# Kernel tuning notes

Measured on AMD Instinct MI355X. Metric: run time of the kernel, lower is better.

## Reference

```python
import jax, jax.numpy as jnp
import numpy as np

EPS_NORM = 1e-12
BN_EPS = 1e-5
TEMP = 0.07


def _l2norm(x, axis):
    n = jnp.sqrt(jnp.sum(x * x, axis=axis, keepdims=True))
    return x / jnp.maximum(n, EPS_NORM)


def _bn_eval(z, w, b):
    # inference-mode BatchNorm2d with running_mean=0, running_var=1
    s = w / jnp.sqrt(jnp.asarray(1.0 + BN_EPS, z.dtype))
    return z * s[None, :, None, None] + b[None, :, None, None]


def setup_inputs() -> dict:
    key = jax.random.key(0)
    ks = jax.random.split(key, 8)
    B, C, H, W = 16, 256, 64, 64
    KD, P = 128, 256
    x = jax.random.normal(ks[0], (B, C, H, W), jnp.float32)
    m_features = jax.random.normal(ks[1], (P, KD), jnp.float32)
    q_w = jax.random.normal(ks[2], (KD, C), jnp.float32) * 0.05
    k_w = jax.random.normal(ks[3], (KD, KD), jnp.float32) * 0.05
    v_w = jax.random.normal(ks[4], (KD, KD), jnp.float32) * 0.05
    o_w = jax.random.normal(ks[5], (C, KD), jnp.float32) * 0.05
    dw_w = jax.random.normal(ks[6], (C, 1, 3, 3), jnp.float32) * 0.1
    return {
        "x": x, "m_features": m_features,
        "q_w": q_w, "q_b": jnp.zeros((KD,), jnp.float32),
        "k_w": k_w, "k_b": jnp.zeros((KD,), jnp.float32),
        "v_w": v_w, "v_b": jnp.zeros((KD,), jnp.float32),
        "o_w": o_w, "o_b": jnp.zeros((C,), jnp.float32),
        "dw_w": dw_w,
        "bn1_w": jnp.ones((C,), jnp.float32), "bn1_b": jnp.zeros((C,), jnp.float32),
        "bn2_w": jnp.ones((C,), jnp.float32), "bn2_b": jnp.zeros((C,), jnp.float32),
        "gamma": jnp.ones((C,), jnp.float32) * 1e-5,
    }


def reference(x, m_features, q_w, q_b, k_w, k_b, v_w, v_b, o_w, o_b,
              dw_w, bn1_w, bn1_b, bn2_w, bn2_b, gamma):
    B, C, H, W = x.shape
    KD = q_w.shape[0]
    residual = x
    # q_proj 1x1 conv -> [B,KD,H,W], L2-normalize over channel dim
    q = jnp.einsum('bchw,kc->bkhw', x, q_w) + q_b[None, :, None, None]
    q = _l2norm(q, axis=1)
    q = q.reshape(B, KD, H * W).transpose(0, 2, 1)  # [B, HW, KD]
    # k/v projections of memory bank [P, KD]
    k = _l2norm(m_features @ k_w.T + k_b, axis=-1)
    v = m_features @ v_w.T + v_b
    # fp32 attention with clamped logits
    q32, k32, v32 = q.astype(jnp.float32), k.astype(jnp.float32), v.astype(jnp.float32)
    logits = jnp.clip(jnp.einsum('bnd,pd->bnp', q32, k32) / TEMP, -30.0, 30.0)
    attn = jax.nn.softmax(logits, axis=-1)
    out = jnp.einsum('bnp,pd->bnd', attn, v32).astype(x.dtype)
    out = out.transpose(0, 2, 1).reshape(B, KD, H, W)
    # out_proj 1x1 conv -> [B,C,H,W]
    out = jnp.einsum('bkhw,ck->bchw', out, o_w) + o_b[None, :, None, None]
    # local branch: depthwise 3x3 conv + BN + exact GELU
    local = jax.lax.conv_general_dilated(
        out, dw_w, window_strides=(1, 1), padding='SAME',
        feature_group_count=C,
        dimension_numbers=('NCHW', 'OIHW', 'NCHW'))
    local = jax.nn.gelu(_bn_eval(local, bn1_w, bn1_b), approximate=False)
    out = out + local
    return _bn_eval(residual + out * gamma[None, :, None, None], bn2_w, bn2_b)
```

## Files before the change

### kernel.cpp

```cpp
#include <hip/hip_runtime.h>
#include <hip/hip_bf16.h>
#include <math.h>

#define B_ 16
#define C_ 256
#define H_ 64
#define W_ 64
#define KD_ 128
#define P_ 256
#define HW_ (H_ * W_)

typedef __bf16 bf16;
typedef bf16 bf16x8_t __attribute__((ext_vector_type(8)));
typedef float f32x4_t __attribute__((ext_vector_type(4)));
typedef float f32x16_t __attribute__((ext_vector_type(16)));
typedef unsigned char u8;

__device__ __forceinline__ unsigned cvt_pk_fp8_lo(float a, float b, unsigned old) {
#if __has_builtin(__builtin_amdgcn_cvt_pk_fp8_f32)
    return __builtin_amdgcn_cvt_pk_fp8_f32(a, b, old, false);
#else
    unsigned r = old;
    asm("v_cvt_pk_fp8_f32 %0, %1, %2" : "+v"(r) : "v"(a), "v"(b));
    return r;
#endif
}
__device__ __forceinline__ unsigned cvt_pk_fp8_hi(float a, float b, unsigned old) {
#if __has_builtin(__builtin_amdgcn_cvt_pk_fp8_f32)
    return __builtin_amdgcn_cvt_pk_fp8_f32(a, b, old, true);
#else
    unsigned r = old;
    asm("v_cvt_pk_fp8_f32 %0, %1, %2 op_sel:[0,0,1]" : "+v"(r) : "v"(a), "v"(b));
    return r;
#endif
}
__device__ __forceinline__ uint2 pack8_fp8(const float* f) {
    uint2 r;
    r.x = cvt_pk_fp8_hi(f[2], f[3], cvt_pk_fp8_lo(f[0], f[1], 0u));
    r.y = cvt_pk_fp8_hi(f[6], f[7], cvt_pk_fp8_lo(f[4], f[5], 0u));
    return r;
}

__global__ __launch_bounds__(512, 8) void k_xpose(
    const float* __restrict__ x, u8* __restrict__ x8)
{
    __shared__ __align__(16) u8 tile[16 * 2048];
    const int cblk = blockIdx.x >> 1;
    const int ph   = blockIdx.x & 1;
    const int b    = blockIdx.y;
    const int t = threadIdx.x;

    {
        const int cl = t >> 5, sub = t & 31;
        const float* src = x + ((size_t)b * C_ + cblk * 16 + cl) * HW_ + ph * 2048;
#pragma unroll
        for (int i = 0; i < 16; ++i) {
            const f32x4_t v = *(const f32x4_t*)(src + (i * 32 + sub) * 4);
            const unsigned w = cvt_pk_fp8_hi(v[2], v[3],
                               cvt_pk_fp8_lo(v[0], v[1], 0u));
            *(unsigned*)&tile[cl * 2048 + (i * 32 + sub) * 4] = w;
        }
    }
    __syncthreads();

    {
        const int pr = t & 63;
        const int r0 = t >> 6;
#pragma unroll
        for (int it = 0; it < 4; ++it) {
            const int r = it * 8 + r0;
            const int lp = r * 64 + pr;
            union { u8 bytes[16]; uint4 u; } g;
#pragma unroll
            for (int c = 0; c < 16; ++c) g.bytes[c] = tile[c * 2048 + lp];
            const int h = ph * 32 + r;
            *(uint4*)(x8 + (((size_t)(b * 64 + h) * 16 + cblk) << 10) + pr * 16) = g.u;
        }
    }
}

__global__ __launch_bounds__(128) void k_prep1(
    const float* __restrict__ m_feat,
    const float* __restrict__ k_w, const float* __restrict__ k_b,
    const float* __restrict__ v_w, const float* __restrict__ v_b,
    float* __restrict__ kn_f, float* __restrict__ v_f)
{
    const int p = blockIdx.x;
    const int j = threadIdx.x;
    __shared__ float msh[KD_];
    __shared__ float red[2];
    msh[j] = m_feat[p * KD_ + j];
    __syncthreads();

    float ka = k_b[j];
    float va = v_b[j];
#pragma unroll 4
    for (int d = 0; d < KD_; ++d) {
        const float m = msh[d];
        ka = fmaf(m, k_w[j * KD_ + d], ka);
        va = fmaf(m, v_w[j * KD_ + d], va);
    }
    float s = ka * ka;
#pragma unroll
    for (int o = 1; o < 64; o <<= 1) s += __shfl_xor(s, o);
    if ((j & 63) == 0) red[j >> 6] = s;
    __syncthreads();
    s = red[0] + red[1];
    const float inv = 1.0f / (0.07f * fmaxf(sqrtf(s), 1e-12f));
    kn_f[p * KD_ + j] = ka * inv;
    v_f[p * KD_ + j] = va;
}

__global__ __launch_bounds__(256) void k_prep23(
    const float* __restrict__ o_w, const float* __restrict__ v_f,
    const float* __restrict__ q_w, const float* __restrict__ kn_f,
    u8* __restrict__ m28, u8* __restrict__ qw8, u8* __restrict__ kn8)
{
    if (blockIdx.x < 256) {
        const int c = blockIdx.x;
        const int p = threadIdx.x;
        __shared__ float osh[KD_];
        if (p < KD_) osh[p] = o_w[c * KD_ + p];
        __syncthreads();
        float acc = 0.f;
#pragma unroll 4
        for (int k = 0; k < KD_; ++k) acc = fmaf(osh[k], v_f[p * KD_ + k], acc);
        const int mt = c >> 5, r = c & 31;
        const int ks = p >> 4, sub = (p >> 3) & 1, jj = p & 7;
        const unsigned pk = cvt_pk_fp8_lo(acc * 16.0f, 0.f, 0u);
        m28[(((mt * 16 + ks) * 64) + sub * 32 + r) * 8 + jj] = (u8)(pk & 0xffu);
    } else {
        const int t = (blockIdx.x - 256) * 256 + threadIdx.x;
        float f[8];
        if (t < 4096) {
            const int lane = t & 63, g = t >> 6, mt = g >> 4, ks = g & 15;
            const int row = mt * 32 + (lane & 31), k0 = ks * 16 + (lane >> 5) * 8;
            const float* src = q_w + row * C_ + k0;
#pragma unroll
            for (int j = 0; j < 8; ++j) f[j] = src[j] * 16.0f;
            ((uint2*)qw8)[t] = pack8_fp8(f);
        } else {
            const int u = t - 4096;
            const int lane = u & 63, g = u >> 6, mt = g >> 3, ks = g & 7;
            const int row = mt * 32 + (lane & 31), k0 = ks * 16 + (lane >> 5) * 8;
            const float* src = kn_f + row * KD_ + k0;
#pragma unroll
            for (int j = 0; j < 8; ++j) f[j] = src[j];
            ((uint2*)kn8)[u] = pack8_fp8(f);
        }
    }
}

__global__ __launch_bounds__(512, 8) void k_attn(
    const u8* __restrict__ x8,
    const float* __restrict__ q_b, const float* __restrict__ o_b,
    const u8* __restrict__ qw8, const u8* __restrict__ kn8,
    const u8* __restrict__ m28, bf16* __restrict__ outf)
{
    __shared__ __align__(16) char lds[29696];
    char* const ebuf = lds;
    char* const qbuf = lds + 16384;
    float* const ss_lds   = (float*)(lds + 24576);
    float* const pmax_lds = (float*)(lds + 25600);
    float* const sum_lds  = (float*)(lds + 27648);

    const int h = blockIdx.x;
    const int b = blockIdx.y;
    const int tid = threadIdx.x;
    const int lane = tid & 63;
    const int wid = tid >> 6;
    const int l31 = lane & 31;
    const int kh  = lane >> 5;

    const int mtA = wid & 3, nhalf = wid >> 2;
    {
        const u8* xrow = x8 + ((size_t)(b * 64 + h) << 14);
        f32x16_t qacc;
#pragma unroll
        for (int i = 0; i < 16; ++i) qacc[i] = 0.f;
        const int pix = nhalf * 32 + l31;
#pragma unroll
        for (int ks = 0; ks < 16; ++ks) {
            const long a = *(const long*)(qw8 + ((mtA * 16 + ks) * 64 + lane) * 8);
            const long bx = *(const long*)(xrow + ks * 1024 + pix * 16 + kh * 8);
            qacc = __builtin_amdgcn_mfma_f32_32x32x16_fp8_fp8(a, bx, qacc, 0, 0, 0);
        }
        float ssp = 0.f;
#pragma unroll
        for (int g = 0; g < 4; ++g) {
            const f32x4_t qbv = *(const f32x4_t*)(q_b + mtA * 32 + g * 8 + kh * 4);
#pragma unroll
            for (int i = 0; i < 4; ++i) {
                const float qv = qacc[g * 4 + i] + 16.0f * qbv[i];
                qacc[g * 4 + i] = qv;
                ssp = fmaf(qv, qv, ssp);
            }
        }
        ssp += __shfl_xor(ssp, 32);
        if (lane < 32) ss_lds[pix * 4 + mtA] = ssp;
#pragma unroll
        for (int g = 0; g < 4; ++g) {
            const unsigned qw_ = cvt_pk_fp8_hi(qacc[g * 4 + 2], qacc[g * 4 + 3],
                                 cvt_pk_fp8_lo(qacc[g * 4 + 0], qacc[g * 4 + 1], 0u));
            *(unsigned*)(qbuf + pix * 128 +
                         ((mtA * 32 + g * 8 + kh * 4) ^ ((l31 & 15) << 3))) = qw_;
        }
    }
    __syncthreads();

    f32x16_t lacc0, lacc1;
#pragma unroll
    for (int i = 0; i < 16; ++i) { lacc0[i] = 0.f; lacc1[i] = 0.f; }
#pragma unroll
    for (int ks = 0; ks < 8; ++ks) {
        const long a = *(const long*)(kn8 + ((wid * 8 + ks) * 64 + lane) * 8);
        const long bq0 = *(const long*)(qbuf + (0 * 32 + l31) * 128 +
                                        ((ks * 16 + kh * 8) ^ ((l31 & 15) << 3)));
        const long bq1 = *(const long*)(qbuf + (1 * 32 + l31) * 128 +
                                        ((ks * 16 + kh * 8) ^ ((l31 & 15) << 3)));
        lacc0 = __builtin_amdgcn_mfma_f32_32x32x16_fp8_fp8(a, bq0, lacc0, 0, 0, 0);
        lacc1 = __builtin_amdgcn_mfma_f32_32x32x16_fp8_fp8(a, bq1, lacc1, 0, 0, 0);
    }
#pragma unroll
    for (int nt = 0; nt < 2; ++nt) {
        const int pix = nt * 32 + l31;
        float mx;
        if (nt == 0) {
            mx = lacc0[0];
#pragma unroll
            for (int i = 1; i < 16; ++i) mx = fmaxf(mx, lacc0[i]);
        } else {
            mx = lacc1[0];
#pragma unroll
            for (int i = 1; i < 16; ++i) mx = fmaxf(mx, lacc1[i]);
        }
        mx = fmaxf(mx, __shfl_xor(mx, 32));
        if (lane < 32) pmax_lds[pix * 8 + wid] = mx;
    }
    __syncthreads();

#pragma unroll
    for (int nt = 0; nt < 2; ++nt) {
        const int pix = nt * 32 + l31;
        const f32x4_t s4 = *(const f32x4_t*)(ss_lds + pix * 4);
        const float qinv = 1.0f / fmaxf(sqrtf(s4[0] + s4[1] + s4[2] + s4[3]), 1e-12f);
        const f32x4_t ma = *(const f32x4_t*)(pmax_lds + pix * 8);
        const f32x4_t mb = *(const f32x4_t*)(pmax_lds + pix * 8 + 4);
        const float cof = 5.545177444479562f -
                          fmaxf(fmaxf(fmaxf(ma[0], ma[1]), fmaxf(ma[2], ma[3])),
                                fmaxf(fmaxf(mb[0], mb[1]), fmaxf(mb[2], mb[3]))) * qinv;
        float sm = 0.f;
#pragma unroll
        for (int g = 0; g < 4; ++g) {
            float e[4];
#pragma unroll
            for (int i = 0; i < 4; ++i) {
                const float lv = (nt == 0) ? lacc0[g * 4 + i] : lacc1[g * 4 + i];
                e[i] = __expf(fmaf(lv, qinv, cof));
                sm += e[i];
            }
            const unsigned ew = cvt_pk_fp8_hi(e[2], e[3],
                                cvt_pk_fp8_lo(e[0], e[1], 0u));
            const int p0 = wid * 32 + g * 8 + kh * 4;
            *(unsigned*)(ebuf + pix * 256 + (p0 ^ (l31 << 3))) = ew;
        }
        sm += __shfl_xor(sm, 32);
        if (lane < 32) sum_lds[pix * 8 + wid] = sm;
    }
    __syncthreads();

    f32x16_t oacc0, oacc1;
#pragma unroll
    for (int i = 0; i < 16; ++i) { oacc0[i] = 0.f; oacc1[i] = 0.f; }
#pragma unroll
    for (int ks = 0; ks < 16; ++ks) {
        const long a = *(const long*)(m28 + ((wid * 16 + ks) * 64 + lane) * 8);
        const long be0 = *(const long*)(ebuf + (0 * 32 + l31) * 256 +
                                        ((ks * 16 + kh * 8) ^ (l31 << 3)));
        const long be1 = *(const long*)(ebuf + (1 * 32 + l31) * 256 +
                                        ((ks * 16 + kh * 8) ^ (l31 << 3)));
        oacc0 = __builtin_amdgcn_mfma_f32_32x32x16_fp8_fp8(a, be0, oacc0, 0, 0, 0);
        oacc1 = __builtin_amdgcn_mfma_f32_32x32x16_fp8_fp8(a, be1, oacc1, 0, 0, 0);
    }
    {
        const f32x4_t sa0 = *(const f32x4_t*)(sum_lds + (0 * 32 + l31) * 8);
        const f32x4_t sb0 = *(const f32x4_t*)(sum_lds + (0 * 32 + l31) * 8 + 4);
        const f32x4_t sa1 = *(const f32x4_t*)(sum_lds + (1 * 32 + l31) * 8);
        const f32x4_t sb1 = *(const f32x4_t*)(sum_lds + (1 * 32 + l31) * 8 + 4);
        const float rs0 = 1.0f / (16.0f * (sa0[0] + sa0[1] + sa0[2] + sa0[3] +
                                           sb0[0] + sb0[1] + sb0[2] + sb0[3]));
        const float rs1 = 1.0f / (16.0f * (sa1[0] + sa1[1] + sa1[2] + sa1[3] +
                                           sb1[0] + sb1[1] + sb1[2] + sb1[3]));
        bf16* const obase = outf + (size_t)b * C_ * HW_ + h * W_;
#pragma unroll
        for (int g = 0; g < 4; ++g) {
            const f32x4_t obv = *(const f32x4_t*)(o_b + wid * 32 + g * 8 + kh * 4);
#pragma unroll
            for (int i = 0; i < 4; ++i) {
                const int c = wid * 32 + g * 8 + kh * 4 + i;
                obase[(size_t)c * HW_ + l31]      = (bf16)fmaf(oacc0[g * 4 + i], rs0, obv[i]);
                obase[(size_t)c * HW_ + 32 + l31] = (bf16)fmaf(oacc1[g * 4 + i], rs1, obv[i]);
            }
        }
    }
}

__global__ __launch_bounds__(256) void k_post(
    const float* __restrict__ x, const bf16* __restrict__ outf,
    const float* __restrict__ dw_w,
    const float* __restrict__ bn1_w, const float* __restrict__ bn1_b,
    const float* __restrict__ bn2_w, const float* __restrict__ bn2_b,
    const float* __restrict__ gamma, float* __restrict__ y)
{
    __shared__ __align__(16) bf16 os[HW_];
    const int bc = blockIdx.x;
    const int c = bc & (C_ - 1);
    const int tid = threadIdx.x;

    const bf16* oc = outf + (size_t)bc * HW_;
#pragma unroll
    for (int it = 0; it < 2; ++it) {
        const int e = (it * 256 + tid) * 8;
        *(bf16x8_t*)&os[e] = *(const bf16x8_t*)&oc[e];
    }

    const float cbn = 0.99999500003750f;
    const float s1 = bn1_w[c] * cbn, b1 = bn1_b[c];
    const float s2 = bn2_w[c] * cbn, b2 = bn2_b[c];
    const float g = gamma[c];
    float kw[9];
#pragma unroll
    for (int j = 0; j < 9; ++j) kw[j] = dw_w[c * 9 + j];

    __syncthreads();

    const int w = tid & 63;
    const int h0 = (tid >> 6) * 16;

    float r0[3], r1[3], r2[3];
    auto ldrow = [&](int hh, float* r) {
        if ((unsigned)hh < (unsigned)H_) {
            r[1] = (float)os[hh * W_ + w];
            r[0] = (w > 0) ? (float)os[hh * W_ + w - 1] : 0.f;
            r[2] = (w < W_ - 1) ? (float)os[hh * W_ + w + 1] : 0.f;
        } else {
            r[0] = r[1] = r[2] = 0.f;
        }
    };
    ldrow(h0 - 1, r0);
    ldrow(h0, r1);

    const float* xc = x + (size_t)bc * HW_;
    float* yc = y + (size_t)bc * HW_;

#pragma unroll
    for (int i = 0; i < 16; ++i) {
        const int h = h0 + i;
        ldrow(h + 1, r2);
        float conv = kw[0] * r0[0];
        conv = fmaf(kw[1], r0[1], conv);
        conv = fmaf(kw[2], r0[2], conv);
        conv = fmaf(kw[3], r1[0], conv);
        conv = fmaf(kw[4], r1[1], conv);
        conv = fmaf(kw[5], r1[2], conv);
        conv = fmaf(kw[6], r2[0], conv);
        conv = fmaf(kw[7], r2[1], conv);
        conv = fmaf(kw[8], r2[2], conv);
        const float center = r1[1];
        const float t = fmaf(conv, s1, b1);
        const float lg = t / (1.0f + __expf(-1.702f * t));
        const int idx = h * W_ + w;
        yc[idx] = fmaf(center + lg, g, xc[idx]) * s2 + b2;
#pragma unroll
        for (int j = 0; j < 3; ++j) { r0[j] = r1[j]; r1[j] = r2[j]; }
    }
}

extern "C" void kernel_launch(void* const* d_in, const int* in_sizes, int n_in,
                              void* d_out, int out_size, void* d_ws, size_t ws_size,
                              hipStream_t stream)
{
    const float* x     = (const float*)d_in[0];
    const float* m_f   = (const float*)d_in[1];
    const float* q_w   = (const float*)d_in[2];
    const float* q_b   = (const float*)d_in[3];
    const float* k_w   = (const float*)d_in[4];
    const float* k_b   = (const float*)d_in[5];
    const float* v_w   = (const float*)d_in[6];
    const float* v_b   = (const float*)d_in[7];
    const float* o_w   = (const float*)d_in[8];
    const float* o_b   = (const float*)d_in[9];
    const float* dw_w  = (const float*)d_in[10];
    const float* bn1_w = (const float*)d_in[11];
    const float* bn1_b = (const float*)d_in[12];
    const float* bn2_w = (const float*)d_in[13];
    const float* bn2_b = (const float*)d_in[14];
    const float* gamma = (const float*)d_in[15];

    char* ws = (char*)d_ws;
    u8*    qw8   = (u8*)(ws);
    u8*    kn8   = (u8*)(ws + (32 << 10));
    u8*    m28   = (u8*)(ws + (64 << 10));
    u8*    x8    = (u8*)(ws + (1 << 20));
    bf16*  outf  = (bf16*)(ws + (17 << 20));
    float* kn_f  = (float*)(ws + (17 << 20));
    float* v_f   = (float*)(ws + (17 << 20) + (128 << 10));

    k_xpose<<<dim3(32, B_), dim3(512), 0, stream>>>(x, x8);
    k_prep1<<<dim3(P_), dim3(128), 0, stream>>>(m_f, k_w, k_b, v_w, v_b,
                                                kn_f, v_f);
    k_prep23<<<dim3(288), dim3(256), 0, stream>>>(o_w, v_f, q_w, kn_f,
                                                  m28, qw8, kn8);
    k_attn<<<dim3(H_, B_), dim3(512), 0, stream>>>(x8, q_b, o_b, qw8, kn8,
                                                   m28, outf);
    k_post<<<dim3(B_ * C_), dim3(256), 0, stream>>>(
        x, outf, dw_w, bn1_w, bn1_b, bn2_w, bn2_b, gamma, (float*)d_out);
}
```

Before: 87.09 us.

## Process two rows per attention block and pass fp8 intermediate to post kernel

The attention kernel now handles two image rows (128 pixels) per block, so each wave reuses its loaded K/V/weight fragments across four MFMA tiles instead of two, and the grid is halved. The attention output is stored as fp8, scaled by 16, instead of bf16, which halves the intermediate traffic. The post kernel is rewritten to load that fp8 into padded LDS, decode it, and compute four contiguous pixels per thread with vectorized x loads and y stores. The cost is higher register/LDS pressure per block and extra precision loss in the residual branch.

```diff
diff --git a/kernel.cpp b/kernel.cpp
--- a/kernel.cpp
+++ b/kernel.cpp
@@ -11,7 +11,6 @@
 #define HW_ (H_ * W_)
 
 typedef __bf16 bf16;
-typedef bf16 bf16x8_t __attribute__((ext_vector_type(8)));
 typedef float f32x4_t __attribute__((ext_vector_type(4)));
 typedef float f32x16_t __attribute__((ext_vector_type(16)));
 typedef unsigned char u8;
@@ -40,6 +39,16 @@
     r.y = cvt_pk_fp8_hi(f[6], f[7], cvt_pk_fp8_lo(f[4], f[5], 0u));
     return r;
 }
+template<int SEL>
+__device__ __forceinline__ float fp8_to_f32(unsigned w) {
+#if __has_builtin(__builtin_amdgcn_cvt_f32_fp8)
+    return __builtin_amdgcn_cvt_f32_fp8(w, SEL);
+#else
+    float r;
+    asm("v_cvt_f32_fp8 %0, %1" : "=v"(r) : "v"(w >> (SEL * 8)));
+    return r;
+#endif
+}
 
 __global__ __launch_bounds__(512, 8) void k_xpose(
     const float* __restrict__ x, u8* __restrict__ x8)
@@ -62,7 +71,6 @@
         }
     }
     __syncthreads();
-
     {
         const int pr = t & 63;
         const int r0 = t >> 6;
@@ -151,20 +159,20 @@
     }
 }
 
-__global__ __launch_bounds__(512, 8) void k_attn(
+__global__ __launch_bounds__(512, 4) void k_attn(
     const u8* __restrict__ x8,
     const float* __restrict__ q_b, const float* __restrict__ o_b,
     const u8* __restrict__ qw8, const u8* __restrict__ kn8,
-    const u8* __restrict__ m28, bf16* __restrict__ outf)
-{
-    __shared__ __align__(16) char lds[29696];
+    const u8* __restrict__ m28, u8* __restrict__ outf8)
+{
+    __shared__ __align__(16) char lds[43008];
     char* const ebuf = lds;
     char* const qbuf = lds + 16384;
-    float* const ss_lds   = (float*)(lds + 24576);
-    float* const pmax_lds = (float*)(lds + 25600);
-    float* const sum_lds  = (float*)(lds + 27648);
-
-    const int h = blockIdx.x;
+    float* const ss_lds   = (float*)(lds + 32768);
+    float* const pmax_lds = (float*)(lds + 34816);
+    float* const sum_lds  = (float*)(lds + 38912);
+
+    const int rp = blockIdx.x;
     const int b = blockIdx.y;
     const int tid = threadIdx.x;
     const int lane = tid & 63;
@@ -172,67 +180,76 @@
     const int l31 = lane & 31;
     const int kh  = lane >> 5;
 
-    const int mtA = wid & 3, nhalf = wid >> 2;
+    const int mtA = wid & 3, nh = wid >> 2;
     {
-        const u8* xrow = x8 + ((size_t)(b * 64 + h) << 14);
-        f32x16_t qacc;
-#pragma unroll
-        for (int i = 0; i < 16; ++i) qacc[i] = 0.f;
-        const int pix = nhalf * 32 + l31;
+        const u8* xrow = x8 + ((size_t)(b * 64 + rp * 2 + nh) << 14);
+        f32x16_t qacc0, qacc1;
+#pragma unroll
+        for (int i = 0; i < 16; ++i) { qacc0[i] = 0.f; qacc1[i] = 0.f; }
 #pragma unroll
         for (int ks = 0; ks < 16; ++ks) {
             const long a = *(const long*)(qw8 + ((mtA * 16 + ks) * 64 + lane) * 8);
-            const long bx = *(const long*)(xrow + ks * 1024 + pix * 16 + kh * 8);
-            qacc = __builtin_amdgcn_mfma_f32_32x32x16_fp8_fp8(a, bx, qacc, 0, 0, 0);
-        }
-        float ssp = 0.f;
-#pragma unroll
-        for (int g = 0; g < 4; ++g) {
-            const f32x4_t qbv = *(const f32x4_t*)(q_b + mtA * 32 + g * 8 + kh * 4);
-#pragma unroll
-            for (int i = 0; i < 4; ++i) {
-                const float qv = qacc[g * 4 + i] + 16.0f * qbv[i];
-                qacc[g * 4 + i] = qv;
-                ssp = fmaf(qv, qv, ssp);
+            const long bx0 = *(const long*)(xrow + ks * 1024 + l31 * 16 + kh * 8);
+            const long bx1 = *(const long*)(xrow + ks * 1024 + (32 + l31) * 16 + kh * 8);
+            qacc0 = __builtin_amdgcn_mfma_f32_32x32x16_fp8_fp8(a, bx0, qacc0, 0, 0, 0);
+            qacc1 = __builtin_amdgcn_mfma_f32_32x32x16_fp8_fp8(a, bx1, qacc1, 0, 0, 0);
+        }
+#pragma unroll
+        for (int nt = 0; nt < 2; ++nt) {
+            const int pix = nh * 64 + nt * 32 + l31;
+            float ssp = 0.f;
+#pragma unroll
+            for (int g = 0; g < 4; ++g) {
+                const f32x4_t qbv = *(const f32x4_t*)(q_b + mtA * 32 + g * 8 + kh * 4);
+#pragma unroll
+                for (int i = 0; i < 4; ++i) {
+                    float qv = (nt == 0) ? qacc0[g * 4 + i] : qacc1[g * 4 + i];
+                    qv += 16.0f * qbv[i];
+                    if (nt == 0) qacc0[g * 4 + i] = qv; else qacc1[g * 4 + i] = qv;
+                    ssp = fmaf(qv, qv, ssp);
+                }
             }
-        }
-        ssp += __shfl_xor(ssp, 32);
-        if (lane < 32) ss_lds[pix * 4 + mtA] = ssp;
-#pragma unroll
-        for (int g = 0; g < 4; ++g) {
-            const unsigned qw_ = cvt_pk_fp8_hi(qacc[g * 4 + 2], qacc[g * 4 + 3],
-                                 cvt_pk_fp8_lo(qacc[g * 4 + 0], qacc[g * 4 + 1], 0u));
-            *(unsigned*)(qbuf + pix * 128 +
-                         ((mtA * 32 + g * 8 + kh * 4) ^ ((l31 & 15) << 3))) = qw_;
-        }
-    }
-    __syncthreads();
-
-    f32x16_t lacc0, lacc1;
-#pragma unroll
-    for (int i = 0; i < 16; ++i) { lacc0[i] = 0.f; lacc1[i] = 0.f; }
+            ssp += __shfl_xor(ssp, 32);
+            if (lane < 32) ss_lds[pix * 4 + mtA] = ssp;
+#pragma unroll
+            for (int g = 0; g < 4; ++g) {
+                const float e0 = (nt == 0) ? qacc0[g * 4 + 0] : qacc1[g * 4 + 0];
+                const float e1 = (nt == 0) ? qacc0[g * 4 + 1] : qacc1[g * 4 + 1];
+                const float e2 = (nt == 0) ? qacc0[g * 4 + 2] : qacc1[g * 4 + 2];
+                const float e3 = (nt == 0) ? qacc0[g * 4 + 3] : qacc1[g * 4 + 3];
+                const unsigned qw_ = cvt_pk_fp8_hi(e2, e3, cvt_pk_fp8_lo(e0, e1, 0u));
+                *(unsigned*)(qbuf + pix * 128 +
+                             ((mtA * 32 + g * 8 + kh * 4) ^ ((l31 & 15) << 3))) = qw_;
+            }
+        }
+    }
+    __syncthreads();
+
+    f32x16_t lacc0, lacc1, lacc2, lacc3;
+#pragma unroll
+    for (int i = 0; i < 16; ++i) { lacc0[i] = 0.f; lacc1[i] = 0.f; lacc2[i] = 0.f; lacc3[i] = 0.f; }
 #pragma unroll
     for (int ks = 0; ks < 8; ++ks) {
         const long a = *(const long*)(kn8 + ((wid * 8 + ks) * 64 + lane) * 8);
-        const long bq0 = *(const long*)(qbuf + (0 * 32 + l31) * 128 +
-                                        ((ks * 16 + kh * 8) ^ ((l31 & 15) << 3)));
-        const long bq1 = *(const long*)(qbuf + (1 * 32 + l31) * 128 +
-                                        ((ks * 16 + kh * 8) ^ ((l31 & 15) << 3)));
+        const int ko = (ks * 16 + kh * 8) ^ ((l31 & 15) << 3);
+        const long bq0 = *(const long*)(qbuf + (0 * 32 + l31) * 128 + ko);
+        const long bq1 = *(const long*)(qbuf + (1 * 32 + l31) * 128 + ko);
+        const long bq2 = *(const long*)(qbuf + (2 * 32 + l31) * 128 + ko);
+        const long bq3 = *(const long*)(qbuf + (3 * 32 + l31) * 128 + ko);
         lacc0 = __builtin_amdgcn_mfma_f32_32x32x16_fp8_fp8(a, bq0, lacc0, 0, 0, 0);
         lacc1 = __builtin_amdgcn_mfma_f32_32x32x16_fp8_fp8(a, bq1, lacc1, 0, 0, 0);
-    }
-#pragma unroll
-    for (int nt = 0; nt < 2; ++nt) {
+        lacc2 = __builtin_amdgcn_mfma_f32_32x32x16_fp8_fp8(a, bq2, lacc2, 0, 0, 0);
+        lacc3 = __builtin_amdgcn_mfma_f32_32x32x16_fp8_fp8(a, bq3, lacc3, 0, 0, 0);
+    }
+#pragma unroll
+    for (int nt = 0; nt < 4; ++nt) {
         const int pix = nt * 32 + l31;
-        float mx;
-        if (nt == 0) {
-            mx = lacc0[0];
-#pragma unroll
-            for (int i = 1; i < 16; ++i) mx = fmaxf(mx, lacc0[i]);
-        } else {
-            mx = lacc1[0];
-#pragma unroll
-            for (int i = 1; i < 16; ++i) mx = fmaxf(mx, lacc1[i]);
+        float mx = -1e30f;
+#pragma unroll
+        for (int i = 0; i < 16; ++i) {
+            const float lv = (nt == 0) ? lacc0[i] : (nt == 1) ? lacc1[i]
+                           : (nt == 2) ? lacc2[i] : lacc3[i];
+            mx = fmaxf(mx, lv);
         }
         mx = fmaxf(mx, __shfl_xor(mx, 32));
         if (lane < 32) pmax_lds[pix * 8 + wid] = mx;
@@ -240,7 +257,7 @@
     __syncthreads();
 
 #pragma unroll
-    for (int nt = 0; nt < 2; ++nt) {
+    for (int nt = 0; nt < 4; ++nt) {
         const int pix = nt * 32 + l31;
         const f32x4_t s4 = *(const f32x4_t*)(ss_lds + pix * 4);
         const float qinv = 1.0f / fmaxf(sqrtf(s4[0] + s4[1] + s4[2] + s4[3]), 1e-12f);
@@ -255,7 +272,8 @@
             float e[4];
 #pragma unroll
             for (int i = 0; i < 4; ++i) {
-                const float lv = (nt == 0) ? lacc0[g * 4 + i] : lacc1[g * 4 + i];
+                const float lv = (nt == 0) ? lacc0[g * 4 + i] : (nt == 1) ? lacc1[g * 4 + i]
+                               : (nt == 2) ? lacc2[g * 4 + i] : lacc3[g * 4 + i];
                 e[i] = __expf(fmaf(lv, qinv, cof));
                 sm += e[i];
             }
@@ -269,110 +287,137 @@
     }
     __syncthreads();
 
-    f32x16_t oacc0, oacc1;
-#pragma unroll
-    for (int i = 0; i < 16; ++i) { oacc0[i] = 0.f; oacc1[i] = 0.f; }
+    f32x16_t oacc0, oacc1, oacc2, oacc3;
+#pragma unroll
+    for (int i = 0; i < 16; ++i) { oacc0[i] = 0.f; oacc1[i] = 0.f; oacc2[i] = 0.f; oacc3[i] = 0.f; }
 #pragma unroll
     for (int ks = 0; ks < 16; ++ks) {
         const long a = *(const long*)(m28 + ((wid * 16 + ks) * 64 + lane) * 8);
-        const long be0 = *(const long*)(ebuf + (0 * 32 + l31) * 256 +
-                                        ((ks * 16 + kh * 8) ^ (l31 << 3)));
-        const long be1 = *(const long*)(ebuf + (1 * 32 + l31) * 256 +
-                                        ((ks * 16 + kh * 8) ^ (l31 << 3)));
+        const int ko = (ks * 16 + kh * 8);
+        const long be0 = *(const long*)(ebuf + (0 * 32 + l31) * 256 + (ko ^ (l31 << 3)));
+        const long be1 = *(const long*)(ebuf + (1 * 32 + l31) * 256 + (ko ^ (l31 << 3)));
+        const long be2 = *(const long*)(ebuf + (2 * 32 + l31) * 256 + (ko ^ (l31 << 3)));
+        const long be3 = *(const long*)(ebuf + (3 * 32 + l31) * 256 + (ko ^ (l31 << 3)));
         oacc0 = __builtin_amdgcn_mfma_f32_32x32x16_fp8_fp8(a, be0, oacc0, 0, 0, 0);
         oacc1 = __builtin_amdgcn_mfma_f32_32x32x16_fp8_fp8(a, be1, oacc1, 0, 0, 0);
+        oacc2 = __builtin_amdgcn_mfma_f32_32x32x16_fp8_fp8(a, be2, oacc2, 0, 0, 0);
+        oacc3 = __builtin_amdgcn_mfma_f32_32x32x16_fp8_fp8(a, be3, oacc3, 0, 0, 0);
     }
     {
-        const f32x4_t sa0 = *(const f32x4_t*)(sum_lds + (0 * 32 + l31) * 8);
-        const f32x4_t sb0 = *(const f32x4_t*)(sum_lds + (0 * 32 + l31) * 8 + 4);
-        const f32x4_t sa1 = *(const f32x4_t*)(sum_lds + (1 * 32 + l31) * 8);
-        const f32x4_t sb1 = *(const f32x4_t*)(sum_lds + (1 * 32 + l31) * 8 + 4);
-        const float rs0 = 1.0f / (16.0f * (sa0[0] + sa0[1] + sa0[2] + sa0[3] +
-                                           sb0[0] + sb0[1] + sb0[2] + sb0[3]));
-        const float rs1 = 1.0f / (16.0f * (sa1[0] + sa1[1] + sa1[2] + sa1[3] +
-                                           sb1[0] + sb1[1] + sb1[2] + sb1[3]));
-        bf16* const obase = outf + (size_t)b * C_ * HW_ + h * W_;
+        u8* const obase = outf8 + (size_t)b * C_ * HW_ + rp * 128;
+        f32x4_t obv16[4];
 #pragma unroll
         for (int g = 0; g < 4; ++g) {
-            const f32x4_t obv = *(const f32x4_t*)(o_b + wid * 32 + g * 8 + kh * 4);
-#pragma unroll
-            for (int i = 0; i < 4; ++i) {
-                const int c = wid * 32 + g * 8 + kh * 4 + i;
-                obase[(size_t)c * HW_ + l31]      = (bf16)fmaf(oacc0[g * 4 + i], rs0, obv[i]);
-                obase[(size_t)c * HW_ + 32 + l31] = (bf16)fmaf(oacc1[g * 4 + i], rs1, obv[i]);
+            const f32x4_t t = *(const f32x4_t*)(o_b + wid * 32 + g * 8 + kh * 4);
+            obv16[g] = t * 16.0f;
+        }
+#pragma unroll
+        for (int nt = 0; nt < 4; ++nt) {
+            const int p = nt * 32 + l31;
+            const f32x4_t sa = *(const f32x4_t*)(sum_lds + p * 8);
+            const f32x4_t sb = *(const f32x4_t*)(sum_lds + p * 8 + 4);
+            const float rs16 = 1.0f / ((sa[0] + sa[1] + sa[2] + sa[3]) +
+                                       (sb[0] + sb[1] + sb[2] + sb[3]));
+            u8* const op = obase + p;
+#pragma unroll
+            for (int g = 0; g < 4; ++g) {
+                float o[4];
+#pragma unroll
+                for (int i = 0; i < 4; ++i) {
+                    const float av = (nt == 0) ? oacc0[g * 4 + i] : (nt == 1) ? oacc1[g * 4 + i]
+                                   : (nt == 2) ? oacc2[g * 4 + i] : oacc3[g * 4 + i];
+                    o[i] = fmaf(av, rs16, obv16[g][i]);
+                }
+                const unsigned u01 = cvt_pk_fp8_lo(o[0], o[1], 0u);
+                const unsigned u23 = cvt_pk_fp8_lo(o[2], o[3], 0u);
+                const int c = wid * 32 + g * 8 + kh * 4;
+                op[(size_t)(c + 0) * HW_] = (u8)(u01 & 0xff);
+                op[(size_t)(c + 1) * HW_] = (u8)((u01 >> 8) & 0xff);
+                op[(size_t)(c + 2) * HW_] = (u8)(u23 & 0xff);
+                op[(size_t)(c + 3) * HW_] = (u8)((u23 >> 8) & 0xff);
             }
         }
     }
 }
 
-__global__ __launch_bounds__(256) void k_post(
-    const float* __restrict__ x, const bf16* __restrict__ outf,
+__global__ __launch_bounds__(256, 4) void k_post(
+    const float* __restrict__ x, const u8* __restrict__ outf8,
     const float* __restrict__ dw_w,
     const float* __restrict__ bn1_w, const float* __restrict__ bn1_b,
     const float* __restrict__ bn2_w, const float* __restrict__ bn2_b,
     const float* __restrict__ gamma, float* __restrict__ y)
 {
-    __shared__ __align__(16) bf16 os[HW_];
+    __shared__ __align__(16) u8 os8[64 + HW_ + 64];
+    u8* const os = os8 + 64;
     const int bc = blockIdx.x;
     const int c = bc & (C_ - 1);
     const int tid = threadIdx.x;
 
-    const bf16* oc = outf + (size_t)bc * HW_;
-#pragma unroll
-    for (int it = 0; it < 2; ++it) {
-        const int e = (it * 256 + tid) * 8;
-        *(bf16x8_t*)&os[e] = *(const bf16x8_t*)&oc[e];
-    }
+    if (tid < 4)       *(uint4*)&os8[tid * 16] = make_uint4(0, 0, 0, 0);
+    else if (tid < 8)  *(uint4*)&os8[64 + HW_ + (tid - 4) * 16] = make_uint4(0, 0, 0, 0);
+    *(uint4*)&os[tid * 16] = *(const uint4*)(outf8 + (size_t)bc * HW_ + tid * 16);
 
     const float cbn = 0.99999500003750f;
     const float s1 = bn1_w[c] * cbn, b1 = bn1_b[c];
     const float s2 = bn2_w[c] * cbn, b2 = bn2_b[c];
     const float g = gamma[c];
+    const float gc = g * 0.0625f;
     float kw[9];
 #pragma unroll
-    for (int j = 0; j < 9; ++j) kw[j] = dw_w[c * 9 + j];
-
-    __syncthreads();
-
-    const int w = tid & 63;
-    const int h0 = (tid >> 6) * 16;
-
-    float r0[3], r1[3], r2[3];
-    auto ldrow = [&](int hh, float* r) {
-        if ((unsigned)hh < (unsigned)H_) {
-            r[1] = (float)os[hh * W_ + w];
-            r[0] = (w > 0) ? (float)os[hh * W_ + w - 1] : 0.f;
-            r[2] = (w < W_ - 1) ? (float)os[hh * W_ + w + 1] : 0.f;
-        } else {
-            r[0] = r[1] = r[2] = 0.f;
-        }
-    };
-    ldrow(h0 - 1, r0);
-    ldrow(h0, r1);
-
+    for (int j = 0; j < 9; ++j) kw[j] = dw_w[c * 9 + j] * 0.0625f;
+
+    __syncthreads();
+
+    const int q = tid & 15;
+    const int c4 = q * 4;
+    const int r0 = tid >> 4;
     const float* xc = x + (size_t)bc * HW_;
     float* yc = y + (size_t)bc * HW_;
 
 #pragma unroll
-    for (int i = 0; i < 16; ++i) {
-        const int h = h0 + i;
-        ldrow(h + 1, r2);
-        float conv = kw[0] * r0[0];
-        conv = fmaf(kw[1], r0[1], conv);
-        conv = fmaf(kw[2], r0[2], conv);
-        conv = fmaf(kw[3], r1[0], conv);
-        conv = fmaf(kw[4], r1[1], conv);
-        conv = fmaf(kw[5], r1[2], conv);
-        conv = fmaf(kw[6], r2[0], conv);
-        conv = fmaf(kw[7], r2[1], conv);
-        conv = fmaf(kw[8], r2[2], conv);
-        const float center = r1[1];
-        const float t = fmaf(conv, s1, b1);
-        const float lg = t / (1.0f + __expf(-1.702f * t));
-        const int idx = h * W_ + w;
-        yc[idx] = fmaf(center + lg, g, xc[idx]) * s2 + b2;
-#pragma unroll
-        for (int j = 0; j < 3; ++j) { r0[j] = r1[j]; r1[j] = r2[j]; }
+    for (int k = 0; k < 4; ++k) {
+        const int r = r0 + k * 16;
+        const f32x4_t x4 = *(const f32x4_t*)(xc + r * 64 + c4);
+        float vt[6], vm[6], vb[6];
+        {
+            const int rbt = r * 64, rbm = rbt + 64, rbb = rbt + 128;
+            const unsigned uCt = *(const unsigned*)&os8[rbt + c4];
+            const unsigned uCm = *(const unsigned*)&os8[rbm + c4];
+            const unsigned uCb = *(const unsigned*)&os8[rbb + c4];
+            vt[1] = fp8_to_f32<0>(uCt); vt[2] = fp8_to_f32<1>(uCt);
+            vt[3] = fp8_to_f32<2>(uCt); vt[4] = fp8_to_f32<3>(uCt);
+            vm[1] = fp8_to_f32<0>(uCm); vm[2] = fp8_to_f32<1>(uCm);
+            vm[3] = fp8_to_f32<2>(uCm); vm[4] = fp8_to_f32<3>(uCm);
+            vb[1] = fp8_to_f32<0>(uCb); vb[2] = fp8_to_f32<1>(uCb);
+            vb[3] = fp8_to_f32<2>(uCb); vb[4] = fp8_to_f32<3>(uCb);
+            if (q > 0) {
+                vt[0] = fp8_to_f32<3>(*(const unsigned*)&os8[rbt + c4 - 4]);
+                vm[0] = fp8_to_f32<3>(*(const unsigned*)&os8[rbm + c4 - 4]);
+                vb[0] = fp8_to_f32<3>(*(const unsigned*)&os8[rbb + c4 - 4]);
+            } else { vt[0] = vm[0] = vb[0] = 0.f; }
+            if (q < 15) {
+                vt[5] = fp8_to_f32<0>(*(const unsigned*)&os8[rbt + c4 + 4]);
+                vm[5] = fp8_to_f32<0>(*(const unsigned*)&os8[rbm + c4 + 4]);
+                vb[5] = fp8_to_f32<0>(*(const unsigned*)&os8[rbb + c4 + 4]);
+            } else { vt[5] = vm[5] = vb[5] = 0.f; }
+        }
+        f32x4_t y4;
+#pragma unroll
+        for (int j = 0; j < 4; ++j) {
+            float conv = kw[0] * vt[j];
+            conv = fmaf(kw[1], vt[j + 1], conv);
+            conv = fmaf(kw[2], vt[j + 2], conv);
+            conv = fmaf(kw[3], vm[j], conv);
+            conv = fmaf(kw[4], vm[j + 1], conv);
+            conv = fmaf(kw[5], vm[j + 2], conv);
+            conv = fmaf(kw[6], vb[j], conv);
+            conv = fmaf(kw[7], vb[j + 1], conv);
+            conv = fmaf(kw[8], vb[j + 2], conv);
+            const float t = fmaf(conv, s1, b1);
+            const float lg = t / (1.0f + __expf(-1.702f * t));
+            y4[j] = fmaf(lg, g, fmaf(vm[j + 1], gc, x4[j])) * s2 + b2;
+        }
+        *(f32x4_t*)(yc + r * 64 + c4) = y4;
     }
 }
 
@@ -402,17 +447,17 @@
     u8*    kn8   = (u8*)(ws + (32 << 10));
     u8*    m28   = (u8*)(ws + (64 << 10));
     u8*    x8    = (u8*)(ws + (1 << 20));
-    bf16*  outf  = (bf16*)(ws + (17 << 20));
-    float* kn_f  = (float*)(ws + (17 << 20));
-    float* v_f   = (float*)(ws + (17 << 20) + (128 << 10));
+    u8*    outf8 = (u8*)(ws + (17 << 20));
+    float* kn_f  = (float*)(ws + (34 << 20));
+    float* v_f   = (float*)(ws + (34 << 20) + (128 << 10));
 
     k_xpose<<<dim3(32, B_), dim3(512), 0, stream>>>(x, x8);
     k_prep1<<<dim3(P_), dim3(128), 0, stream>>>(m_f, k_w, k_b, v_w, v_b,
                                                 kn_f, v_f);
     k_prep23<<<dim3(288), dim3(256), 0, stream>>>(o_w, v_f, q_w, kn_f,
                                                   m28, qw8, kn8);
-    k_attn<<<dim3(H_, B_), dim3(512), 0, stream>>>(x8, q_b, o_b, qw8, kn8,
-                                                   m28, outf);
+    k_attn<<<dim3(H_ / 2, B_), dim3(512), 0, stream>>>(x8, q_b, o_b, qw8, kn8,
+                                                       m28, outf8);
     k_post<<<dim3(B_ * C_), dim3(256), 0, stream>>>(
-        x, outf, dw_w, bn1_w, bn1_b, bn2_w, bn2_b, gamma, (float*)d_out);
-}
+        x, outf8, dw_w, bn1_w, bn1_b, bn2_w, bn2_b, gamma, (float*)d_out);
+}
```

Result: faster. 81.25 us (-6.7%).
